# Kernel optimization log

Measured on AMD Instinct MI355X. Metric: run time of the kernel, lower is better.

The kernel has to match this reference:

```python
import jax, jax.numpy as jnp
import numpy as np

B, N, H = 2, 2048, 256
NUM_HEADS = 8
HEAD_DIM = H // NUM_HEADS
E = 65536
NEG = -1e30
LN_EPS = 1e-5


def setup_inputs() -> dict:
    key = jax.random.key(0)
    ks = jax.random.split(key, 8)
    x = jax.random.normal(ks[0], (B, N, H), dtype=jnp.float32)
    edge_index = jax.random.randint(ks[1], (2, E), 0, N, dtype=jnp.int32)
    edge_weights = jax.random.uniform(ks[2], (E,), dtype=jnp.float32)
    s = 1.0 / np.sqrt(H)
    Wq = jax.random.normal(ks[3], (H, H), dtype=jnp.float32) * s
    Wk = jax.random.normal(ks[4], (H, H), dtype=jnp.float32) * s
    Wv = jax.random.normal(ks[5], (H, H), dtype=jnp.float32) * s
    Wo = jax.random.normal(ks[6], (H, H), dtype=jnp.float32) * s
    ln_gamma = jnp.ones((H,), dtype=jnp.float32)
    ln_beta = jnp.zeros((H,), dtype=jnp.float32)
    return {"node_embeddings": x, "edge_index": edge_index, "edge_weights": edge_weights,
            "Wq": Wq, "Wk": Wk, "Wv": Wv, "Wo": Wo, "ln_gamma": ln_gamma, "ln_beta": ln_beta}


def reference(node_embeddings, edge_index, edge_weights, Wq, Wk, Wv, Wo, ln_gamma, ln_beta):
    x = node_embeddings
    residual = x
    # torch Linear: y = x @ W.T
    def proj(W):
        y = jnp.einsum('bnd,ed->bne', x, W)
        return y.reshape(B, N, NUM_HEADS, HEAD_DIM).transpose(0, 2, 1, 3)  # [B,h,N,hd]
    Q, K, V = proj(Wq), proj(Wk), proj(Wv)
    scale = 1.0 / jnp.sqrt(jnp.float32(HEAD_DIM))
    scores = jnp.einsum('bhnd,bhmd->bhnm', Q, K) * scale  # [B,h,N,N]
    # adjacency mask from edge list
    mask = jnp.zeros((N, N), dtype=bool).at[edge_index[0], edge_index[1]].set(True)
    scores = jnp.where(mask[None, None], scores, NEG)
    w = jax.nn.softmax(scores, axis=-1)
    # rows with no edges: softmax over uniform NEG -> uniform; multiply by mask zeroes them
    # (equivalent to torch's -inf softmax + nan->0, but grad-safe)
    w = w * mask[None, None].astype(w.dtype)
    attn = jnp.einsum('bhnm,bhmd->bhnd', w, V)
    attn = attn.transpose(0, 2, 1, 3).reshape(B, N, H)
    out = jnp.einsum('bnd,ed->bne', attn, Wo)
    y = out + residual
    mu = jnp.mean(y, axis=-1, keepdims=True)
    var = jnp.mean(jnp.square(y - mu), axis=-1, keepdims=True)
    y = (y - mu) / jnp.sqrt(var + LN_EPS) * ln_gamma + ln_beta
    return y
```

## Files before the change

kernel.cpp:

```cpp
#include <hip/hip_runtime.h>
#include <math.h>

#define Bb 2
#define Nn 2048
#define Hh 256
#define NH 8
#define HD 32
#define NEDGE 65536
#define LN_EPS 1e-5f
#define MW 64
#define LDA2 72

typedef __bf16 bf16_t;
typedef bf16_t bf16x8 __attribute__((ext_vector_type(8)));
typedef bf16_t bf16x4 __attribute__((ext_vector_type(4)));
typedef float f32x4 __attribute__((ext_vector_type(4)));

__global__ __launch_bounds__(256) void prep_kernel(
    const float* __restrict__ x,
    const float* __restrict__ Wq, const float* __restrict__ Wk, const float* __restrict__ Wv,
    float* __restrict__ Qb, bf16_t* __restrict__ Kb16, bf16_t* __restrict__ Vb16,
    unsigned int* __restrict__ mask)
{
    __shared__ bf16_t As[64 * LDA2];
    __shared__ bf16_t Ws[64 * LDA2];
    const int u = blockIdx.x;
    const int t = threadIdx.x;

    if (u >= 768) {
        uint4* m4 = (uint4*)mask;
        const uint4 z = make_uint4(0, 0, 0, 0);
        int b0 = (u - 768) * 1024 + t;
        #pragma unroll
        for (int r = 0; r < 4; ++r) m4[b0 + r * 256] = z;
        return;
    }

    const int lane = t & 63, w = t >> 6;
    const int wm = w & 1, wn = w >> 1;
    const int ml = lane & 15, quad = lane >> 4;
    const int m0 = (u & 63) << 6;
    const int ysel = u >> 6;
    const int wsel = ysel >> 2;
    const float* W = (wsel == 0) ? Wq : ((wsel == 1) ? Wk : Wv);
    const int n0 = (ysel & 3) << 6;
    const int srow = t >> 3, scol = (t & 7) * 8;
    f32x4 acc[2][2];
    f32x4 zero = {0.f, 0.f, 0.f, 0.f};
    acc[0][0] = zero; acc[0][1] = zero; acc[1][0] = zero; acc[1][1] = zero;

    for (int k0 = 0; k0 < Hh; k0 += 64) {
        float4 a[2][2], bwt[2][2];
        #pragma unroll
        for (int s = 0; s < 2; ++s) {
            const float* ap = x + (size_t)(m0 + srow + s * 32) * Hh + k0 + scol;
            a[s][0] = *(const float4*)ap;
            a[s][1] = *(const float4*)(ap + 4);
            const float* bp = W + (size_t)(n0 + srow + s * 32) * Hh + k0 + scol;
            bwt[s][0] = *(const float4*)bp;
            bwt[s][1] = *(const float4*)(bp + 4);
        }
        __syncthreads();
        #pragma unroll
        for (int s = 0; s < 2; ++s) {
            bf16x8 av = {(bf16_t)a[s][0].x, (bf16_t)a[s][0].y, (bf16_t)a[s][0].z, (bf16_t)a[s][0].w,
                         (bf16_t)a[s][1].x, (bf16_t)a[s][1].y, (bf16_t)a[s][1].z, (bf16_t)a[s][1].w};
            bf16x8 bv = {(bf16_t)bwt[s][0].x, (bf16_t)bwt[s][0].y, (bf16_t)bwt[s][0].z, (bf16_t)bwt[s][0].w,
                         (bf16_t)bwt[s][1].x, (bf16_t)bwt[s][1].y, (bf16_t)bwt[s][1].z, (bf16_t)bwt[s][1].w};
            *(bf16x8*)&As[(srow + s * 32) * LDA2 + scol] = av;
            *(bf16x8*)&Ws[(srow + s * 32) * LDA2 + scol] = bv;
        }
        __syncthreads();
        #pragma unroll
        for (int kk = 0; kk < 64; kk += 32) {
            bf16x8 af[2], bfr[2];
            #pragma unroll
            for (int i = 0; i < 2; ++i) {
                af[i]  = *(const bf16x8*)&As[(wm * 32 + i * 16 + ml) * LDA2 + kk + quad * 8];
                bfr[i] = *(const bf16x8*)&Ws[(wn * 32 + i * 16 + ml) * LDA2 + kk + quad * 8];
            }
            #pragma unroll
            for (int i = 0; i < 2; ++i)
                #pragma unroll
                for (int j = 0; j < 2; ++j)
                    acc[i][j] = __builtin_amdgcn_mfma_f32_16x16x32_bf16(af[i], bfr[j], acc[i][j], 0, 0, 0);
        }
    }
    bf16_t* Ob16 = (wsel == 1) ? Kb16 : Vb16;
    #pragma unroll
    for (int i = 0; i < 2; ++i)
        #pragma unroll
        for (int j = 0; j < 2; ++j)
            #pragma unroll
            for (int r = 0; r < 4; ++r) {
                int mg = m0 + wm * 32 + i * 16 + quad * 4 + r;
                int ng = n0 + wn * 32 + j * 16 + ml;
                float v = acc[i][j][r];
                if (wsel == 0) Qb[(size_t)mg * Hh + ng] = v;
                else           Ob16[(size_t)mg * Hh + ng] = (bf16_t)v;
            }
}

__global__ void build_mask_kernel(const int* __restrict__ ei, unsigned int* __restrict__ mask) {
    int e = blockIdx.x * blockDim.x + threadIdx.x;
    if (e >= NEDGE) return;
    int src = ei[e];
    int dst = ei[NEDGE + e];
    atomicOr(&mask[src * MW + (dst >> 5)], 1u << (dst & 31));
}

__global__ __launch_bounds__(256) void attn7_kernel(
    const float* __restrict__ Qb, const bf16_t* __restrict__ Kb16, const bf16_t* __restrict__ Vb16,
    const unsigned int* __restrict__ mask, float* __restrict__ attnb)
{
    __shared__ unsigned short nbr[4][2048];
    const int t = threadIdx.x;
    const int w = t >> 6, lane = t & 63;
    const int i = (blockIdx.x << 1) + (w >> 1);
    const int b = w & 1;

    unsigned int bits = mask[i * MW + lane];
    int cnt = __popc(bits);
    int incl = cnt;
    #pragma unroll
    for (int off = 1; off < 64; off <<= 1) {
        int v = __shfl_up(incl, off, 64);
        if (lane >= off) incl += v;
    }
    int idx = incl - cnt;
    unsigned int bb = bits;
    while (bb) {
        int bit = __ffs(bb) - 1;
        nbr[w][idx++] = (unsigned short)(lane * 32 + bit);
        bb &= bb - 1;
    }
    int nn = __shfl(incl, 63, 64);
    if (lane == 63) nbr[w][idx] = 0;
    __syncthreads();

    const int off4 = lane << 2;
    const float4 qv = *(const float4*)(Qb + (size_t)((b << 11) + i) * Hh + off4);
    const bf16_t* kb = Kb16 + (((size_t)(b << 11)) << 8);
    const bf16_t* vb = Vb16 + (((size_t)(b << 11)) << 8);
    const float scale = 0.17677669529663687f;

    float m_run = -1e30f, l_run = 0.f;
    float o0 = 0.f, o1 = 0.f, o2 = 0.f, o3 = 0.f;
    if (nn > 0) {
        int j = nbr[w][0];
        bf16x4 kv = *(const bf16x4*)(kb + ((size_t)j << 8) + off4);
        bf16x4 vv = *(const bf16x4*)(vb + ((size_t)j << 8) + off4);
        for (int n = 0; n < nn; ++n) {
            int jn = nbr[w][n + 1];
            bf16x4 kn = *(const bf16x4*)(kb + ((size_t)jn << 8) + off4);
            bf16x4 vn = *(const bf16x4*)(vb + ((size_t)jn << 8) + off4);
            float p = fmaf((float)kv.x, qv.x, fmaf((float)kv.y, qv.y,
                      fmaf((float)kv.z, qv.z, (float)kv.w * qv.w)));
            p += __shfl_xor(p, 1, 64);
            p += __shfl_xor(p, 2, 64);
            p += __shfl_xor(p, 4, 64);
            p *= scale;
            float m_new = fmaxf(m_run, p);
            float alpha = __expf(m_run - m_new);
            float wgt   = __expf(p - m_new);
            l_run = fmaf(l_run, alpha, wgt);
            o0 = fmaf(o0, alpha, wgt * (float)vv.x);
            o1 = fmaf(o1, alpha, wgt * (float)vv.y);
            o2 = fmaf(o2, alpha, wgt * (float)vv.z);
            o3 = fmaf(o3, alpha, wgt * (float)vv.w);
            m_run = m_new;
            kv = kn; vv = vn;
        }
    }
    float linv = (l_run > 0.f) ? 1.f / l_run : 0.f;
    float4 ov = {o0 * linv, o1 * linv, o2 * linv, o3 * linv};
    *(float4*)(attnb + ((size_t)((b << 11) + i) << 8) + off4) = ov;
}

__global__ __launch_bounds__(256) void out_ln_kernel(
    const float* __restrict__ attnb, const float* __restrict__ Wo,
    const float* __restrict__ x, const float* __restrict__ gamma,
    const float* __restrict__ beta, float* __restrict__ out)
{
    __shared__ bf16_t As[16 * LDA2];
    __shared__ __align__(16) char wbuf[256 * LDA2 * sizeof(bf16_t)];
    bf16_t* Ws = (bf16_t*)wbuf;
    float* yb = (float*)wbuf;
    int t = threadIdx.x;
    int lane = t & 63, w = t >> 6;
    int ml = lane & 15, quad = lane >> 4;
    int m0 = blockIdx.x * 16;
    f32x4 acc[4];
    f32x4 zero = {0.f, 0.f, 0.f, 0.f};
    acc[0] = zero; acc[1] = zero; acc[2] = zero; acc[3] = zero;
    int arow = t >> 4, acol = (t & 15) * 4;
    int wrow = t >> 3, wcol = (t & 7) * 8;

    for (int k0 = 0; k0 < Hh; k0 += 64) {
        float4 av = *(const float4*)(attnb + (size_t)(m0 + arow) * Hh + k0 + acol);
        float4 wva[8], wvb[8];
        #pragma unroll
        for (int s = 0; s < 8; ++s) {
            const float* wp = Wo + (size_t)(wrow + s * 32) * Hh + k0 + wcol;
            wva[s] = *(const float4*)wp;
            wvb[s] = *(const float4*)(wp + 4);
        }
        __syncthreads();
        bf16x4 ac = {(bf16_t)av.x, (bf16_t)av.y, (bf16_t)av.z, (bf16_t)av.w};
        *(bf16x4*)&As[arow * LDA2 + acol] = ac;
        #pragma unroll
        for (int s = 0; s < 8; ++s) {
            bf16x8 wv8 = {(bf16_t)wva[s].x, (bf16_t)wva[s].y, (bf16_t)wva[s].z, (bf16_t)wva[s].w,
                          (bf16_t)wvb[s].x, (bf16_t)wvb[s].y, (bf16_t)wvb[s].z, (bf16_t)wvb[s].w};
            *(bf16x8*)&Ws[(wrow + s * 32) * LDA2 + wcol] = wv8;
        }
        __syncthreads();
        #pragma unroll
        for (int kk = 0; kk < 64; kk += 32) {
            bf16x8 af = *(const bf16x8*)&As[ml * LDA2 + kk + quad * 8];
            #pragma unroll
            for (int ct = 0; ct < 4; ++ct) {
                bf16x8 bfr = *(const bf16x8*)&Ws[(w * 64 + ct * 16 + ml) * LDA2 + kk + quad * 8];
                acc[ct] = __builtin_amdgcn_mfma_f32_16x16x32_bf16(af, bfr, acc[ct], 0, 0, 0);
            }
        }
    }
    __syncthreads();
    #pragma unroll
    for (int ct = 0; ct < 4; ++ct)
        #pragma unroll
        for (int r = 0; r < 4; ++r) {
            int row = quad * 4 + r;
            int col = w * 64 + ct * 16 + ml;
            yb[row * 260 + col] = acc[ct][r] + x[(size_t)(m0 + row) * Hh + col];
        }
    __syncthreads();
    for (int rr = 0; rr < 4; ++rr) {
        int row = w * 4 + rr;
        float4 v = *(const float4*)&yb[row * 260 + lane * 4];
        float sum = v.x + v.y + v.z + v.w;
        #pragma unroll
        for (int m = 1; m < 64; m <<= 1) sum += __shfl_xor(sum, m, 64);
        float mu = sum * (1.f / Hh);
        float4 d = {v.x - mu, v.y - mu, v.z - mu, v.w - mu};
        float ss = d.x * d.x + d.y * d.y + d.z * d.z + d.w * d.w;
        #pragma unroll
        for (int m = 1; m < 64; m <<= 1) ss += __shfl_xor(ss, m, 64);
        float r = rsqrtf(ss * (1.f / Hh) + LN_EPS);
        float4 g  = *(const float4*)(gamma + lane * 4);
        float4 bt = *(const float4*)(beta + lane * 4);
        float4 ov = {d.x * r * g.x + bt.x, d.y * r * g.y + bt.y,
                     d.z * r * g.z + bt.z, d.w * r * g.w + bt.w};
        *(float4*)(out + (size_t)(m0 + row) * Hh + lane * 4) = ov;
    }
}

extern "C" void kernel_launch(void* const* d_in, const int* in_sizes, int n_in,
                              void* d_out, int out_size, void* d_ws, size_t ws_size,
                              hipStream_t stream) {
    const float* x     = (const float*)d_in[0];
    const int*   ei    = (const int*)d_in[1];
    const float* Wq    = (const float*)d_in[3];
    const float* Wk    = (const float*)d_in[4];
    const float* Wv    = (const float*)d_in[5];
    const float* Wo    = (const float*)d_in[6];
    const float* gamma = (const float*)d_in[7];
    const float* beta  = (const float*)d_in[8];
    float* out = (float*)d_out;

    const int NTOK = Bb * Nn * Hh;
    float*  Qb    = (float*)d_ws;
    bf16_t* Kb16  = (bf16_t*)(Qb + NTOK);
    bf16_t* Vb16  = Kb16 + NTOK;
    float*  attnb = (float*)(Vb16 + NTOK);
    unsigned int* mask = (unsigned int*)(attnb + NTOK);

    hipLaunchKernelGGL(prep_kernel, dim3(800), dim3(256), 0, stream,
                       x, Wq, Wk, Wv, Qb, Kb16, Vb16, mask);
    hipLaunchKernelGGL(build_mask_kernel, dim3(NEDGE / 256), dim3(256), 0, stream, ei, mask);
    hipLaunchKernelGGL(attn7_kernel, dim3(Nn / 2), dim3(256), 0, stream,
                       Qb, Kb16, Vb16, mask, attnb);
    hipLaunchKernelGGL(out_ln_kernel, dim3((Bb * Nn) / 16), dim3(256), 0, stream,
                       attnb, Wo, x, gamma, beta, out);
}
```

Before: 116.1 us.

## Fuse attention with output projection and LayerNorm; merge mask build into prep

```diff
diff --git a/kernel.cpp b/kernel.cpp
--- a/kernel.cpp
+++ b/kernel.cpp
@@ -10,6 +10,8 @@
 #define LN_EPS 1e-5f
 #define MW 64
 #define LDA2 72
+#define ALD 264
+#define NBW 2112
 
 typedef __bf16 bf16_t;
 typedef bf16_t bf16x8 __attribute__((ext_vector_type(8)));
@@ -19,6 +21,7 @@
 __global__ __launch_bounds__(256) void prep_kernel(
     const float* __restrict__ x,
     const float* __restrict__ Wq, const float* __restrict__ Wk, const float* __restrict__ Wv,
+    const int* __restrict__ ei,
     float* __restrict__ Qb, bf16_t* __restrict__ Kb16, bf16_t* __restrict__ Vb16,
     unsigned int* __restrict__ mask)
 {
@@ -28,11 +31,10 @@
     const int t = threadIdx.x;
 
     if (u >= 768) {
-        uint4* m4 = (uint4*)mask;
-        const uint4 z = make_uint4(0, 0, 0, 0);
-        int b0 = (u - 768) * 1024 + t;
-        #pragma unroll
-        for (int r = 0; r < 4; ++r) m4[b0 + r * 256] = z;
+        int e = (u - 768) * 256 + t;
+        int src = ei[e];
+        int dst = ei[NEDGE + e];
+        atomicOr(&mask[src * MW + (dst >> 5)], 1u << (dst & 31));
         return;
     }
 
@@ -101,23 +103,24 @@
             }
 }
 
-__global__ void build_mask_kernel(const int* __restrict__ ei, unsigned int* __restrict__ mask) {
-    int e = blockIdx.x * blockDim.x + threadIdx.x;
-    if (e >= NEDGE) return;
-    int src = ei[e];
-    int dst = ei[NEDGE + e];
-    atomicOr(&mask[src * MW + (dst >> 5)], 1u << (dst & 31));
-}
-
-__global__ __launch_bounds__(256) void attn7_kernel(
+__global__ __launch_bounds__(1024) void attn_out_ln_kernel(
     const float* __restrict__ Qb, const bf16_t* __restrict__ Kb16, const bf16_t* __restrict__ Vb16,
-    const unsigned int* __restrict__ mask, float* __restrict__ attnb)
+    const unsigned int* __restrict__ mask, const float* __restrict__ Wo,
+    const float* __restrict__ x, const float* __restrict__ gamma, const float* __restrict__ beta,
+    float* __restrict__ out)
 {
-    __shared__ unsigned short nbr[4][2048];
+    __shared__ __align__(16) char smem[16 * NBW * 2 + 16 * ALD * 2 + 256 * LDA2 * 2];
+    unsigned short* nbr = (unsigned short*)smem;
+    float*  ybuf = (float*)smem;
+    bf16_t* As   = (bf16_t*)(smem + 16 * NBW * 2);
+    bf16_t* Ws   = (bf16_t*)(smem + 16 * NBW * 2 + 16 * ALD * 2);
+
     const int t = threadIdx.x;
     const int w = t >> 6, lane = t & 63;
-    const int i = (blockIdx.x << 1) + (w >> 1);
-    const int b = w & 1;
+    const int ml = lane & 15, quad = lane >> 4;
+    const int g = (blockIdx.x << 4) + w;
+    const int i = g & (Nn - 1);
+    const int b = g >> 11;
 
     unsigned int bits = mask[i * MW + lane];
     int cnt = __popc(bits);
@@ -131,27 +134,27 @@
     unsigned int bb = bits;
     while (bb) {
         int bit = __ffs(bb) - 1;
-        nbr[w][idx++] = (unsigned short)(lane * 32 + bit);
+        nbr[w * NBW + idx++] = (unsigned short)(lane * 32 + bit);
         bb &= bb - 1;
     }
     int nn = __shfl(incl, 63, 64);
-    if (lane == 63) nbr[w][idx] = 0;
+    if (lane == 63) nbr[w * NBW + idx] = 0;
     __syncthreads();
 
     const int off4 = lane << 2;
-    const float4 qv = *(const float4*)(Qb + (size_t)((b << 11) + i) * Hh + off4);
-    const bf16_t* kb = Kb16 + (((size_t)(b << 11)) << 8);
-    const bf16_t* vb = Vb16 + (((size_t)(b << 11)) << 8);
+    const float4 qv = *(const float4*)(Qb + (size_t)g * Hh + off4);
+    const bf16_t* kb = Kb16 + ((size_t)b << 19);
+    const bf16_t* vb = Vb16 + ((size_t)b << 19);
     const float scale = 0.17677669529663687f;
 
     float m_run = -1e30f, l_run = 0.f;
     float o0 = 0.f, o1 = 0.f, o2 = 0.f, o3 = 0.f;
     if (nn > 0) {
-        int j = nbr[w][0];
+        int j = nbr[w * NBW];
         bf16x4 kv = *(const bf16x4*)(kb + ((size_t)j << 8) + off4);
         bf16x4 vv = *(const bf16x4*)(vb + ((size_t)j << 8) + off4);
         for (int n = 0; n < nn; ++n) {
-            int jn = nbr[w][n + 1];
+            int jn = nbr[w * NBW + n + 1];
             bf16x4 kn = *(const bf16x4*)(kb + ((size_t)jn << 8) + off4);
             bf16x4 vn = *(const bf16x4*)(vb + ((size_t)jn << 8) + off4);
             float p = fmaf((float)kv.x, qv.x, fmaf((float)kv.y, qv.y,
@@ -173,71 +176,43 @@
         }
     }
     float linv = (l_run > 0.f) ? 1.f / l_run : 0.f;
-    float4 ov = {o0 * linv, o1 * linv, o2 * linv, o3 * linv};
-    *(float4*)(attnb + ((size_t)((b << 11) + i) << 8) + off4) = ov;
-}
-
-__global__ __launch_bounds__(256) void out_ln_kernel(
-    const float* __restrict__ attnb, const float* __restrict__ Wo,
-    const float* __restrict__ x, const float* __restrict__ gamma,
-    const float* __restrict__ beta, float* __restrict__ out)
-{
-    __shared__ bf16_t As[16 * LDA2];
-    __shared__ __align__(16) char wbuf[256 * LDA2 * sizeof(bf16_t)];
-    bf16_t* Ws = (bf16_t*)wbuf;
-    float* yb = (float*)wbuf;
-    int t = threadIdx.x;
-    int lane = t & 63, w = t >> 6;
-    int ml = lane & 15, quad = lane >> 4;
-    int m0 = blockIdx.x * 16;
-    f32x4 acc[4];
-    f32x4 zero = {0.f, 0.f, 0.f, 0.f};
-    acc[0] = zero; acc[1] = zero; acc[2] = zero; acc[3] = zero;
-    int arow = t >> 4, acol = (t & 15) * 4;
-    int wrow = t >> 3, wcol = (t & 7) * 8;
-
+    bf16x4 arow = {(bf16_t)(o0 * linv), (bf16_t)(o1 * linv),
+                   (bf16_t)(o2 * linv), (bf16_t)(o3 * linv)};
+    *(bf16x4*)&As[w * ALD + off4] = arow;
+    __syncthreads();
+
+    const int wrow = t >> 2, wcol = (t & 3) << 4;
+    f32x4 acc = {0.f, 0.f, 0.f, 0.f};
     for (int k0 = 0; k0 < Hh; k0 += 64) {
-        float4 av = *(const float4*)(attnb + (size_t)(m0 + arow) * Hh + k0 + acol);
-        float4 wva[8], wvb[8];
-        #pragma unroll
-        for (int s = 0; s < 8; ++s) {
-            const float* wp = Wo + (size_t)(wrow + s * 32) * Hh + k0 + wcol;
-            wva[s] = *(const float4*)wp;
-            wvb[s] = *(const float4*)(wp + 4);
-        }
-        __syncthreads();
-        bf16x4 ac = {(bf16_t)av.x, (bf16_t)av.y, (bf16_t)av.z, (bf16_t)av.w};
-        *(bf16x4*)&As[arow * LDA2 + acol] = ac;
-        #pragma unroll
-        for (int s = 0; s < 8; ++s) {
-            bf16x8 wv8 = {(bf16_t)wva[s].x, (bf16_t)wva[s].y, (bf16_t)wva[s].z, (bf16_t)wva[s].w,
-                          (bf16_t)wvb[s].x, (bf16_t)wvb[s].y, (bf16_t)wvb[s].z, (bf16_t)wvb[s].w};
-            *(bf16x8*)&Ws[(wrow + s * 32) * LDA2 + wcol] = wv8;
-        }
+        const float* wp = Wo + (size_t)wrow * Hh + k0 + wcol;
+        float4 w0 = ((const float4*)wp)[0];
+        float4 w1 = ((const float4*)wp)[1];
+        float4 w2 = ((const float4*)wp)[2];
+        float4 w3 = ((const float4*)wp)[3];
+        __syncthreads();
+        bf16x8 lo = {(bf16_t)w0.x, (bf16_t)w0.y, (bf16_t)w0.z, (bf16_t)w0.w,
+                     (bf16_t)w1.x, (bf16_t)w1.y, (bf16_t)w1.z, (bf16_t)w1.w};
+        bf16x8 hi = {(bf16_t)w2.x, (bf16_t)w2.y, (bf16_t)w2.z, (bf16_t)w2.w,
+                     (bf16_t)w3.x, (bf16_t)w3.y, (bf16_t)w3.z, (bf16_t)w3.w};
+        *(bf16x8*)&Ws[wrow * LDA2 + wcol] = lo;
+        *(bf16x8*)&Ws[wrow * LDA2 + wcol + 8] = hi;
         __syncthreads();
         #pragma unroll
         for (int kk = 0; kk < 64; kk += 32) {
-            bf16x8 af = *(const bf16x8*)&As[ml * LDA2 + kk + quad * 8];
-            #pragma unroll
-            for (int ct = 0; ct < 4; ++ct) {
-                bf16x8 bfr = *(const bf16x8*)&Ws[(w * 64 + ct * 16 + ml) * LDA2 + kk + quad * 8];
-                acc[ct] = __builtin_amdgcn_mfma_f32_16x16x32_bf16(af, bfr, acc[ct], 0, 0, 0);
-            }
-        }
+            bf16x8 af  = *(const bf16x8*)&As[ml * ALD + k0 + kk + quad * 8];
+            bf16x8 bfr = *(const bf16x8*)&Ws[(w * 16 + ml) * LDA2 + kk + quad * 8];
+            acc = __builtin_amdgcn_mfma_f32_16x16x32_bf16(af, bfr, acc, 0, 0, 0);
+        }
+    }
+    #pragma unroll
+    for (int r = 0; r < 4; ++r) {
+        int row = quad * 4 + r;
+        int col = (w << 4) + ml;
+        ybuf[row * 260 + col] = acc[r] + x[(size_t)((blockIdx.x << 4) + row) * Hh + col];
     }
     __syncthreads();
-    #pragma unroll
-    for (int ct = 0; ct < 4; ++ct)
-        #pragma unroll
-        for (int r = 0; r < 4; ++r) {
-            int row = quad * 4 + r;
-            int col = w * 64 + ct * 16 + ml;
-            yb[row * 260 + col] = acc[ct][r] + x[(size_t)(m0 + row) * Hh + col];
-        }
-    __syncthreads();
-    for (int rr = 0; rr < 4; ++rr) {
-        int row = w * 4 + rr;
-        float4 v = *(const float4*)&yb[row * 260 + lane * 4];
+    {
+        float4 v = *(const float4*)&ybuf[w * 260 + off4];
         float sum = v.x + v.y + v.z + v.w;
         #pragma unroll
         for (int m = 1; m < 64; m <<= 1) sum += __shfl_xor(sum, m, 64);
@@ -247,11 +222,11 @@
         #pragma unroll
         for (int m = 1; m < 64; m <<= 1) ss += __shfl_xor(ss, m, 64);
         float r = rsqrtf(ss * (1.f / Hh) + LN_EPS);
-        float4 g  = *(const float4*)(gamma + lane * 4);
-        float4 bt = *(const float4*)(beta + lane * 4);
-        float4 ov = {d.x * r * g.x + bt.x, d.y * r * g.y + bt.y,
-                     d.z * r * g.z + bt.z, d.w * r * g.w + bt.w};
-        *(float4*)(out + (size_t)(m0 + row) * Hh + lane * 4) = ov;
+        float4 gm = *(const float4*)(gamma + off4);
+        float4 bt = *(const float4*)(beta + off4);
+        float4 ov = {d.x * r * gm.x + bt.x, d.y * r * gm.y + bt.y,
+                     d.z * r * gm.z + bt.z, d.w * r * gm.w + bt.w};
+        *(float4*)(out + (size_t)g * Hh + off4) = ov;
     }
 }
 
@@ -272,14 +247,11 @@
     float*  Qb    = (float*)d_ws;
     bf16_t* Kb16  = (bf16_t*)(Qb + NTOK);
     bf16_t* Vb16  = Kb16 + NTOK;
-    float*  attnb = (float*)(Vb16 + NTOK);
-    unsigned int* mask = (unsigned int*)(attnb + NTOK);
-
-    hipLaunchKernelGGL(prep_kernel, dim3(800), dim3(256), 0, stream,
-                       x, Wq, Wk, Wv, Qb, Kb16, Vb16, mask);
-    hipLaunchKernelGGL(build_mask_kernel, dim3(NEDGE / 256), dim3(256), 0, stream, ei, mask);
-    hipLaunchKernelGGL(attn7_kernel, dim3(Nn / 2), dim3(256), 0, stream,
-                       Qb, Kb16, Vb16, mask, attnb);
-    hipLaunchKernelGGL(out_ln_kernel, dim3((Bb * Nn) / 16), dim3(256), 0, stream,
-                       attnb, Wo, x, gamma, beta, out);
+    unsigned int* mask = (unsigned int*)(Vb16 + NTOK);
+
+    hipMemsetAsync(mask, 0, Nn * MW * sizeof(unsigned int), stream);
+    hipLaunchKernelGGL(prep_kernel, dim3(1024), dim3(256), 0, stream,
+                       x, Wq, Wk, Wv, ei, Qb, Kb16, Vb16, mask);
+    hipLaunchKernelGGL(attn_out_ln_kernel, dim3((Bb * Nn) / 16), dim3(1024), 0, stream,
+                       Qb, Kb16, Vb16, mask, Wo, x, gamma, beta, out);
 }
```

New measurement: 110.3 us (median of 2 runs). 1.05x faster.
